# Kernel optimization log

Hardware: AMD Instinct MI355X
Metric: run time of the kernel (lower is better)

Reference implementation:

```python
import jax, jax.numpy as jnp
import numpy as np

N_NODES = 50000
N_EDGES = 800000


def setup_inputs() -> dict:
    key = jax.random.key(0)
    ks = jax.random.split(key, 8)
    x = jax.random.normal(ks[0], (N_NODES, 256), dtype=jnp.float32)
    edge_index = jax.random.randint(ks[1], (2, N_EDGES), 0, N_NODES, dtype=jnp.int64)
    edge_weight = jax.random.uniform(ks[2], (N_EDGES,), dtype=jnp.float32)
    # Glorot-style weights for the 3 GCNConv layers: 256->128->64->32
    def glorot(k, fan_in, fan_out):
        s = jnp.sqrt(6.0 / (fan_in + fan_out))
        return jax.random.uniform(k, (fan_in, fan_out), dtype=jnp.float32, minval=-s, maxval=s)
    return {
        "x": x,
        "edge_index": edge_index,
        "edge_weight": edge_weight,
        "W1": glorot(ks[3], 256, 128), "b1": jnp.zeros((128,), jnp.float32),
        "W2": glorot(ks[4], 128, 64),  "b2": jnp.zeros((64,), jnp.float32),
        "W3": glorot(ks[5], 64, 32),   "b3": jnp.zeros((32,), jnp.float32),
    }


def _gcn_forward(x, row, col, ew, params):
    """Stacked GCNConv+ReLU (PyG semantics: add self loops, symmetric norm)."""
    n = x.shape[0]
    loop = jnp.arange(n, dtype=row.dtype)
    row_f = jnp.concatenate([row, loop])            # [E+N] sources
    col_f = jnp.concatenate([col, loop])            # [E+N] targets
    ew_f = jnp.concatenate([ew, jnp.ones((n,), ew.dtype)])
    deg = jax.ops.segment_sum(ew_f, col_f, num_segments=n)
    dinv = jnp.where(deg > 0, jax.lax.rsqrt(deg), 0.0)
    norm = dinv[row_f] * ew_f * dinv[col_f]         # [E+N]
    for W, b in params:
        h = x @ W                                   # [N, d_out] linear first (PyG order)
        msg = h[row_f] * norm[:, None]              # [E+N, d_out] gather + scale
        agg = jax.ops.segment_sum(msg, col_f, num_segments=n)  # scatter-add
        x = jax.nn.relu(agg + b)                    # fused bias + ReLU
    return x


def reference(x, edge_index, edge_weight, W1, b1, W2, b2, W3, b3):
    row, col = edge_index[0], edge_index[1]
    params = [(W1, b1), (W2, b2), (W3, b3)]
    return _gcn_forward(x, row, col, edge_weight, params)
```

## Files before the change

kernel.cpp:

```cpp
#include <hip/hip_runtime.h>
#include <hip/hip_fp16.h>


#define D0 256
#define D1 128
#define D2 64
#define D3 32

#define FIX_SCALE 16777216.0f
#define FIX_INV   (1.0f / 16777216.0f)

typedef _Float16 half8 __attribute__((ext_vector_type(8)));
typedef float floatx4 __attribute__((ext_vector_type(4)));

__global__ void deg_hist_kernel(const int* __restrict__ ei, const float* __restrict__ ew,
                                unsigned long long* __restrict__ pk,
                                int* __restrict__ rank, int E) {
    int e = blockIdx.x * blockDim.x + threadIdx.x;
    if (e < E) {
        int c = ei[E + e];
        unsigned int wfix = (unsigned int)(ew[e] * FIX_SCALE + 0.5f);
        unsigned long long old = atomicAdd(&pk[c], (1ULL << 32) | (unsigned long long)wfix);
        rank[e] = (int)(old >> 32);
    }
}

__global__ __launch_bounds__(256) void scan_reduce(const unsigned long long* __restrict__ pk,
                                                   float* __restrict__ dinv,
                                                   int* __restrict__ cnt,
                                                   int* __restrict__ blockSum, int N) {
    __shared__ int s[256];
    const int t = threadIdx.x;
    const int i = blockIdx.x * 256 + t;
    int v = 0;
    if (i < N) {
        unsigned long long p = pk[i];
        float d = (float)(unsigned int)(p & 0xffffffffULL) * FIX_INV + 1.0f;
        dinv[i] = rsqrtf(d);
        v = (int)(p >> 32);
        cnt[i] = v;
    }
    s[t] = v;
    __syncthreads();
#pragma unroll
    for (int off = 128; off > 0; off >>= 1) {
        if (t < off) s[t] += s[t + off];
        __syncthreads();
    }
    if (t == 0) blockSum[blockIdx.x] = s[0];
}

__global__ __launch_bounds__(256) void scan_blocksums(int* __restrict__ blockSum,
                                                      int* __restrict__ blockOff,
                                                      int* __restrict__ row_ptr_N,
                                                      int B) {
    __shared__ int s[256];
    const int t = threadIdx.x;
    const int v = (t < B) ? blockSum[t] : 0;
    s[t] = v;
    __syncthreads();
#pragma unroll
    for (int off = 1; off < 256; off <<= 1) {
        int u = (t >= off) ? s[t - off] : 0;
        __syncthreads();
        s[t] += u;
        __syncthreads();
    }
    if (t < B) blockOff[t] = s[t] - v;
    if (t == 255) *row_ptr_N = s[255];
}

__global__ __launch_bounds__(256) void scan_apply(const int* __restrict__ cnt,
                                                  const int* __restrict__ blockOff,
                                                  int* __restrict__ row_ptr, int N) {
    __shared__ int s[256];
    const int t = threadIdx.x;
    const int i = blockIdx.x * 256 + t;
    const int v = (i < N) ? cnt[i] : 0;
    s[t] = v;
    __syncthreads();
#pragma unroll
    for (int off = 1; off < 256; off <<= 1) {
        int u = (t >= off) ? s[t - off] : 0;
        __syncthreads();
        s[t] += u;
        __syncthreads();
    }
    if (i < N) row_ptr[i] = s[t] - v + blockOff[blockIdx.x];
}

__global__ void fill_kernel(const int* __restrict__ ei, const float* __restrict__ ew,
                            const float* __restrict__ dinv,
                            const int* __restrict__ row_ptr, const int* __restrict__ rank,
                            int2* __restrict__ pairs, int E) {
    int e = blockIdx.x * blockDim.x + threadIdx.x;
    if (e < E) {
        int r = ei[e];
        int c = ei[E + e];
        float w = dinv[r] * ew[e] * dinv[c];
        pairs[row_ptr[c] + rank[e]] = make_int2(r, __float_as_int(w));
    }
}

template <int K, int DOUT>
__global__ void wcvt_kernel(const float* __restrict__ W, _Float16* __restrict__ Wt) {
    int idx = blockIdx.x * 256 + threadIdx.x;
    if (idx < K * DOUT) {
        int k = idx / DOUT, n = idx % DOUT;
        Wt[n * K + k] = (_Float16)W[idx];
    }
}

__global__ __launch_bounds__(256) void xcvt_kernel(const float* __restrict__ x,
                                                   _Float16* __restrict__ x16, int total) {
    int i = (blockIdx.x * 256 + threadIdx.x) * 8;
    if (i < total) {
        float4 f0 = *(const float4*)&x[i];
        float4 f1 = *(const float4*)&x[i + 4];
        half8 v;
        v[0] = (_Float16)f0.x; v[1] = (_Float16)f0.y;
        v[2] = (_Float16)f0.z; v[3] = (_Float16)f0.w;
        v[4] = (_Float16)f1.x; v[5] = (_Float16)f1.y;
        v[6] = (_Float16)f1.z; v[7] = (_Float16)f1.w;
        *(half8*)&x16[i] = v;
    }
}

template <int K, int BN>
__global__ __launch_bounds__(256) void mfma_gemm(const _Float16* __restrict__ X,
                                                 const _Float16* __restrict__ Wt,
                                                 _Float16* __restrict__ H, int N) {
    constexpr int NC = K / 32;
    constexpr int CG = BN / 32;
    const int w = blockIdx.x * 4 + (threadIdx.x >> 6);
    const int lane = threadIdx.x & 63;
    const int quad = lane >> 4;
    const int m = lane & 15;
    const int cg = w & (CG - 1);
    const int nslab = N >> 4;
    const int stride = (gridDim.x * 4) / CG;
    int slab = w / CG;
    if (slab >= nslab) return;
    const int n0 = cg * 32;

    half8 b0[NC], b1[NC];
#pragma unroll
    for (int c = 0; c < NC; ++c) {
        b0[c] = *(const half8*)&Wt[(size_t)(n0 + m) * K + c * 32 + quad * 8];
        b1[c] = *(const half8*)&Wt[(size_t)(n0 + 16 + m) * K + c * 32 + quad * 8];
    }

    half8 a[NC];
#pragma unroll
    for (int c = 0; c < NC; ++c)
        a[c] = *(const half8*)&X[(size_t)(slab * 16 + m) * K + c * 32 + quad * 8];

    while (true) {
        const int next = slab + stride;
        half8 an[NC];
        if (next < nslab) {
#pragma unroll
            for (int c = 0; c < NC; ++c)
                an[c] = *(const half8*)&X[(size_t)(next * 16 + m) * K + c * 32 + quad * 8];
        }

        floatx4 acc0 = (floatx4){0.f, 0.f, 0.f, 0.f};
        floatx4 acc1 = (floatx4){0.f, 0.f, 0.f, 0.f};
#pragma unroll
        for (int c = 0; c < NC; ++c) {
            acc0 = __builtin_amdgcn_mfma_f32_16x16x32_f16(a[c], b0[c], acc0, 0, 0, 0);
            acc1 = __builtin_amdgcn_mfma_f32_16x16x32_f16(a[c], b1[c], acc1, 0, 0, 0);
        }

        const int r0 = slab * 16 + quad * 4;
#pragma unroll
        for (int r = 0; r < 4; ++r) {
            H[(size_t)(r0 + r) * BN + n0 + m]      = (_Float16)acc0[r];
            H[(size_t)(r0 + r) * BN + n0 + 16 + m] = (_Float16)acc1[r];
        }

        if (next >= nslab) break;
        slab = next;
#pragma unroll
        for (int c = 0; c < NC; ++c) a[c] = an[c];
    }
}

template <int D, typename OUT>
__global__ __launch_bounds__(256) void agg_kernel(const _Float16* __restrict__ H,
                                                  const int* __restrict__ row_ptr,
                                                  const int2* __restrict__ pairs,
                                                  const float* __restrict__ dinv,
                                                  const float* __restrict__ bias,
                                                  OUT* __restrict__ out, int N) {
    constexpr int TPN = D / 8;
    constexpr int NPB = 256 / TPN;
    const int tid = threadIdx.x;
    const int g = tid / TPN;
    const int lane = tid % TPN;
    const int node = blockIdx.x * NPB + g;
    if (node >= N) return;

    const int beg = row_ptr[node];
    const int end = row_ptr[node + 1];
    float acc[8];
#pragma unroll
    for (int j = 0; j < 8; ++j) acc[j] = 0.0f;

    for (int k = beg; k < end; ++k) {
        int2 p = pairs[k];
        float w = __int_as_float(p.y);
        half8 u = *(const half8*)&H[(size_t)p.x * D + lane * 8];
#pragma unroll
        for (int j = 0; j < 8; ++j) acc[j] = fmaf(w, (float)u[j], acc[j]);
    }
    float di = dinv[node];
    float d2 = di * di;
    {
        half8 u = *(const half8*)&H[(size_t)node * D + lane * 8];
#pragma unroll
        for (int j = 0; j < 8; ++j) acc[j] = fmaf(d2, (float)u[j], acc[j]);
    }
    float b[8];
    *(float4*)&b[0] = *(const float4*)&bias[lane * 8];
    *(float4*)&b[4] = *(const float4*)&bias[lane * 8 + 4];
#pragma unroll
    for (int j = 0; j < 8; ++j) acc[j] = fmaxf(acc[j] + b[j], 0.f);

    if constexpr (sizeof(OUT) == 2) {
        half8 o;
#pragma unroll
        for (int j = 0; j < 8; ++j) o[j] = (_Float16)acc[j];
        *(half8*)&out[(size_t)node * D + lane * 8] = o;
    } else {
        float* dst = (float*)&out[(size_t)node * D + lane * 8];
        *(float4*)&dst[0] = make_float4(acc[0], acc[1], acc[2], acc[3]);
        *(float4*)&dst[4] = make_float4(acc[4], acc[5], acc[6], acc[7]);
    }
}

extern "C" void kernel_launch(void* const* d_in, const int* in_sizes, int n_in,
                              void* d_out, int out_size, void* d_ws, size_t ws_size,
                              hipStream_t stream) {
    const float* x   = (const float*)d_in[0];
    const int* ei    = (const int*)d_in[1];
    const float* ew  = (const float*)d_in[2];
    const float* W1  = (const float*)d_in[3];
    const float* b1  = (const float*)d_in[4];
    const float* W2  = (const float*)d_in[5];
    const float* b2  = (const float*)d_in[6];
    const float* W3  = (const float*)d_in[7];
    const float* b3  = (const float*)d_in[8];
    float* out = (float*)d_out;

    const int N = in_sizes[0] / D0;
    const int E = in_sizes[2];
    (void)n_in; (void)out_size; (void)ws_size;

    char* ws = (char*)d_ws;
    size_t off = 0;
    auto carve = [&](size_t bytes) -> void* {
        void* p = (void*)(ws + off);
        off += (bytes + 255) & ~(size_t)255;
        return p;
    };
    unsigned long long* pk = (unsigned long long*)carve((size_t)N * 8);
    float* dinv    = (float*)carve((size_t)N * 4);
    int*   cnt     = (int*)carve((size_t)N * 4);
    int*   row_ptr = (int*)carve((size_t)(N + 1) * 4);
    int*   rank    = (int*)carve((size_t)E * 4);
    int*   bsum    = (int*)carve(256 * 4);
    int*   boff    = (int*)carve(256 * 4);
    int2*  pairs   = (int2*)carve((size_t)E * 8);
    _Float16* Wt1  = (_Float16*)carve((size_t)D0 * D1 * 2);
    _Float16* Wt2  = (_Float16*)carve((size_t)D1 * D2 * 2);
    _Float16* Wt3  = (_Float16*)carve((size_t)D2 * D3 * 2);
    _Float16* x16  = (_Float16*)carve((size_t)N * D0 * 2);
    _Float16* bufH = (_Float16*)carve((size_t)N * D1 * 2);
    _Float16* bufO = (_Float16*)carve((size_t)N * D1 * 2);

    _Float16* h1   = bufH;
    _Float16* out1 = bufO;
    _Float16* h2   = bufH;
    _Float16* out2 = bufO;
    _Float16* h3   = bufH;

    const int eb = (E + 255) / 256;
    const int scanB = (N + 255) / 256;
    const int gB = 768;

    xcvt_kernel<<<(N * D0 / 8 + 255) / 256, 256, 0, stream>>>(x, x16, N * D0);
    wcvt_kernel<D0, D1><<<(D0 * D1 + 255) / 256, 256, 0, stream>>>(W1, Wt1);
    wcvt_kernel<D1, D2><<<(D1 * D2 + 255) / 256, 256, 0, stream>>>(W2, Wt2);
    wcvt_kernel<D2, D3><<<(D2 * D3 + 255) / 256, 256, 0, stream>>>(W3, Wt3);

    hipMemsetAsync(pk, 0, (size_t)N * 8, stream);
    deg_hist_kernel<<<eb, 256, 0, stream>>>(ei, ew, pk, rank, E);
    scan_reduce<<<scanB, 256, 0, stream>>>(pk, dinv, cnt, bsum, N);
    scan_blocksums<<<1, 256, 0, stream>>>(bsum, boff, &row_ptr[N], scanB);
    scan_apply<<<scanB, 256, 0, stream>>>(cnt, boff, row_ptr, N);
    fill_kernel<<<eb, 256, 0, stream>>>(ei, ew, dinv, row_ptr, rank, pairs, E);

    mfma_gemm<D0, D1><<<gB, 256, 0, stream>>>(x16, Wt1, h1, N);
    agg_kernel<D1, _Float16><<<(N + 15) / 16, 256, 0, stream>>>(h1, row_ptr, pairs, dinv, b1, out1, N);

    mfma_gemm<D1, D2><<<gB, 256, 0, stream>>>(out1, Wt2, h2, N);
    agg_kernel<D2, _Float16><<<(N + 31) / 32, 256, 0, stream>>>(h2, row_ptr, pairs, dinv, b2, out2, N);

    mfma_gemm<D2, D3><<<gB, 256, 0, stream>>>(out2, Wt3, h3, N);
    agg_kernel<D3, float><<<(N + 63) / 64, 256, 0, stream>>>(h3, row_ptr, pairs, dinv, b3, out, N);
}
```

Baseline: 296.6 us.

## Fuse prep kernels, merge scan stages, and software-pipeline aggregation gathers

Merges the degree histogram, input fp16 conversion and the three weight transposes into one block-partitioned launch. Folds the block-sum scan into scan_apply, so each block rescans the block sums redundantly and one launch is dropped. Adds a software-pipelined prefetch of edge pairs and feature rows in the aggregation loop to hide gather latency. These cut launch overhead and expose more memory-level parallelism, at the cost of extra registers and clamped redundant loads near the end of each row.

Measured after the change: 269.0 us. 9.3% less time.

```diff
diff --git a/kernel.cpp b/kernel.cpp
--- a/kernel.cpp
+++ b/kernel.cpp
@@ -13,15 +13,51 @@
 typedef _Float16 half8 __attribute__((ext_vector_type(8)));
 typedef float floatx4 __attribute__((ext_vector_type(4)));
 
-__global__ void deg_hist_kernel(const int* __restrict__ ei, const float* __restrict__ ew,
-                                unsigned long long* __restrict__ pk,
-                                int* __restrict__ rank, int E) {
-    int e = blockIdx.x * blockDim.x + threadIdx.x;
-    if (e < E) {
-        int c = ei[E + e];
-        unsigned int wfix = (unsigned int)(ew[e] * FIX_SCALE + 0.5f);
-        unsigned long long old = atomicAdd(&pk[c], (1ULL << 32) | (unsigned long long)wfix);
-        rank[e] = (int)(old >> 32);
+__global__ __launch_bounds__(256) void prep_kernel(
+        const int* __restrict__ ei, const float* __restrict__ ew,
+        unsigned long long* __restrict__ pk, int* __restrict__ rank, int E,
+        const float* __restrict__ x, _Float16* __restrict__ x16, int xElems,
+        const float* __restrict__ W1, _Float16* __restrict__ Wt1,
+        const float* __restrict__ W2, _Float16* __restrict__ Wt2,
+        const float* __restrict__ W3, _Float16* __restrict__ Wt3,
+        int EB, int XB) {
+    const int b = blockIdx.x;
+    const int tid = threadIdx.x;
+    if (b < EB) {
+        int e = b * 256 + tid;
+        if (e < E) {
+            int c = ei[E + e];
+            unsigned int wfix = (unsigned int)(ew[e] * FIX_SCALE + 0.5f);
+            unsigned long long old =
+                atomicAdd(&pk[c], (1ULL << 32) | (unsigned long long)wfix);
+            rank[e] = (int)(old >> 32);
+        }
+    } else if (b < EB + XB) {
+        int i = ((b - EB) * 256 + tid) * 8;
+        if (i < xElems) {
+            float4 f0 = *(const float4*)&x[i];
+            float4 f1 = *(const float4*)&x[i + 4];
+            half8 v;
+            v[0] = (_Float16)f0.x; v[1] = (_Float16)f0.y;
+            v[2] = (_Float16)f0.z; v[3] = (_Float16)f0.w;
+            v[4] = (_Float16)f1.x; v[5] = (_Float16)f1.y;
+            v[6] = (_Float16)f1.z; v[7] = (_Float16)f1.w;
+            *(half8*)&x16[i] = v;
+        }
+    } else {
+        int idx = (b - EB - XB) * 256 + tid;
+        if (idx < D0 * D1) {
+            int k = idx / D1, n = idx % D1;
+            Wt1[n * D0 + k] = (_Float16)W1[idx];
+        } else if (idx < D0 * D1 + D1 * D2) {
+            int j = idx - D0 * D1;
+            int k = j / D2, n = j % D2;
+            Wt2[n * D1 + k] = (_Float16)W2[j];
+        } else if (idx < D0 * D1 + D1 * D2 + D2 * D3) {
+            int j = idx - D0 * D1 - D1 * D2;
+            int k = j / D3, n = j % D3;
+            Wt3[n * D2 + k] = (_Float16)W3[j];
+        }
     }
 }
 
@@ -50,31 +86,22 @@
     if (t == 0) blockSum[blockIdx.x] = s[0];
 }
 
-__global__ __launch_bounds__(256) void scan_blocksums(int* __restrict__ blockSum,
-                                                      int* __restrict__ blockOff,
-                                                      int* __restrict__ row_ptr_N,
-                                                      int B) {
+__global__ __launch_bounds__(256) void scan_apply(const int* __restrict__ cnt,
+                                                  const int* __restrict__ blockSum,
+                                                  int* __restrict__ row_ptr, int N, int B) {
+    __shared__ int bs[256];
     __shared__ int s[256];
     const int t = threadIdx.x;
-    const int v = (t < B) ? blockSum[t] : 0;
-    s[t] = v;
+    bs[t] = (t < B) ? blockSum[t] : 0;
     __syncthreads();
 #pragma unroll
     for (int off = 1; off < 256; off <<= 1) {
-        int u = (t >= off) ? s[t - off] : 0;
-        __syncthreads();
-        s[t] += u;
-        __syncthreads();
-    }
-    if (t < B) blockOff[t] = s[t] - v;
-    if (t == 255) *row_ptr_N = s[255];
-}
-
-__global__ __launch_bounds__(256) void scan_apply(const int* __restrict__ cnt,
-                                                  const int* __restrict__ blockOff,
-                                                  int* __restrict__ row_ptr, int N) {
-    __shared__ int s[256];
-    const int t = threadIdx.x;
+        int u = (t >= off) ? bs[t - off] : 0;
+        __syncthreads();
+        bs[t] += u;
+        __syncthreads();
+    }
+    const int myOff = (blockIdx.x > 0) ? bs[blockIdx.x - 1] : 0;
     const int i = blockIdx.x * 256 + t;
     const int v = (i < N) ? cnt[i] : 0;
     s[t] = v;
@@ -86,7 +113,8 @@
         s[t] += u;
         __syncthreads();
     }
-    if (i < N) row_ptr[i] = s[t] - v + blockOff[blockIdx.x];
+    if (i < N) row_ptr[i] = s[t] - v + myOff;
+    if (blockIdx.x == 0 && t == 0) row_ptr[N] = bs[B - 1];
 }
 
 __global__ void fill_kernel(const int* __restrict__ ei, const float* __restrict__ ew,
@@ -99,30 +127,6 @@
         int c = ei[E + e];
         float w = dinv[r] * ew[e] * dinv[c];
         pairs[row_ptr[c] + rank[e]] = make_int2(r, __float_as_int(w));
-    }
-}
-
-template <int K, int DOUT>
-__global__ void wcvt_kernel(const float* __restrict__ W, _Float16* __restrict__ Wt) {
-    int idx = blockIdx.x * 256 + threadIdx.x;
-    if (idx < K * DOUT) {
-        int k = idx / DOUT, n = idx % DOUT;
-        Wt[n * K + k] = (_Float16)W[idx];
-    }
-}
-
-__global__ __launch_bounds__(256) void xcvt_kernel(const float* __restrict__ x,
-                                                   _Float16* __restrict__ x16, int total) {
-    int i = (blockIdx.x * 256 + threadIdx.x) * 8;
-    if (i < total) {
-        float4 f0 = *(const float4*)&x[i];
-        float4 f1 = *(const float4*)&x[i + 4];
-        half8 v;
-        v[0] = (_Float16)f0.x; v[1] = (_Float16)f0.y;
-        v[2] = (_Float16)f0.z; v[3] = (_Float16)f0.w;
-        v[4] = (_Float16)f1.x; v[5] = (_Float16)f1.y;
-        v[6] = (_Float16)f1.z; v[7] = (_Float16)f1.w;
-        *(half8*)&x16[i] = v;
     }
 }
 
@@ -207,12 +211,22 @@
 #pragma unroll
     for (int j = 0; j < 8; ++j) acc[j] = 0.0f;
 
-    for (int k = beg; k < end; ++k) {
-        int2 p = pairs[k];
-        float w = __int_as_float(p.y);
-        half8 u = *(const half8*)&H[(size_t)p.x * D + lane * 8];
-#pragma unroll
-        for (int j = 0; j < 8; ++j) acc[j] = fmaf(w, (float)u[j], acc[j]);
+    if (end > beg) {
+        const int last = end - 1;
+        int2 p0 = pairs[beg];
+        int2 p1 = pairs[min(beg + 1, last)];
+        int2 p2 = pairs[min(beg + 2, last)];
+        half8 u0 = *(const half8*)&H[(size_t)p0.x * D + lane * 8];
+        half8 u1 = *(const half8*)&H[(size_t)p1.x * D + lane * 8];
+        for (int k = beg; k < end; ++k) {
+            int2 p3 = pairs[min(k + 3, last)];
+            half8 u2 = *(const half8*)&H[(size_t)p2.x * D + lane * 8];
+            float w = __int_as_float(p0.y);
+#pragma unroll
+            for (int j = 0; j < 8; ++j) acc[j] = fmaf(w, (float)u0[j], acc[j]);
+            p0 = p1; p1 = p2; p2 = p3;
+            u0 = u1; u1 = u2;
+        }
     }
     float di = dinv[node];
     float d2 = di * di;
@@ -270,7 +284,6 @@
     int*   row_ptr = (int*)carve((size_t)(N + 1) * 4);
     int*   rank    = (int*)carve((size_t)E * 4);
     int*   bsum    = (int*)carve(256 * 4);
-    int*   boff    = (int*)carve(256 * 4);
     int2*  pairs   = (int2*)carve((size_t)E * 8);
     _Float16* Wt1  = (_Float16*)carve((size_t)D0 * D1 * 2);
     _Float16* Wt2  = (_Float16*)carve((size_t)D1 * D2 * 2);
@@ -286,19 +299,20 @@
     _Float16* h3   = bufH;
 
     const int eb = (E + 255) / 256;
+    const int xElems = N * D0;
+    const int xb = (xElems / 8 + 255) / 256;
+    const int wElems = D0 * D1 + D1 * D2 + D2 * D3;
+    const int wb = (wElems + 255) / 256;
     const int scanB = (N + 255) / 256;
     const int gB = 768;
 
-    xcvt_kernel<<<(N * D0 / 8 + 255) / 256, 256, 0, stream>>>(x, x16, N * D0);
-    wcvt_kernel<D0, D1><<<(D0 * D1 + 255) / 256, 256, 0, stream>>>(W1, Wt1);
-    wcvt_kernel<D1, D2><<<(D1 * D2 + 255) / 256, 256, 0, stream>>>(W2, Wt2);
-    wcvt_kernel<D2, D3><<<(D2 * D3 + 255) / 256, 256, 0, stream>>>(W3, Wt3);
-
     hipMemsetAsync(pk, 0, (size_t)N * 8, stream);
-    deg_hist_kernel<<<eb, 256, 0, stream>>>(ei, ew, pk, rank, E);
+    prep_kernel<<<eb + xb + wb, 256, 0, stream>>>(
+        ei, ew, pk, rank, E, x, x16, xElems,
+        W1, Wt1, W2, Wt2, W3, Wt3, eb, xb);
+
     scan_reduce<<<scanB, 256, 0, stream>>>(pk, dinv, cnt, bsum, N);
-    scan_blocksums<<<1, 256, 0, stream>>>(bsum, boff, &row_ptr[N], scanB);
-    scan_apply<<<scanB, 256, 0, stream>>>(cnt, boff, row_ptr, N);
+    scan_apply<<<scanB, 256, 0, stream>>>(cnt, bsum, row_ptr, N, scanB);
     fill_kernel<<<eb, 256, 0, stream>>>(ei, ew, dinv, row_ptr, rank, pairs, E);
 
     mfma_gemm<D0, D1><<<gB, 256, 0, stream>>>(x16, Wt1, h1, N);
```
